# Kernel optimization log

Hardware: AMD Instinct MI355X
Metric: run time of the kernel (lower is better)

The kernel has to match this reference:

```python
import jax, jax.numpy as jnp
import numpy as np

N, H, W, C = 4, 128, 128, 128
G = 8
GC = C // G
K = 9  # 3x3 deformable kernel
PAD = 1
HIN, WIN = H + 2 * PAD, W + 2 * PAD
EPS = 1e-5
OFFSET_SCALE = 1.0


def ln(x, g, b):
    m = jnp.mean(x, -1, keepdims=True)
    v = jnp.mean((x - m) ** 2, -1, keepdims=True)
    return (x - m) * jax.lax.rsqrt(v + EPS) * g + b


def gelu(x):
    return jax.nn.gelu(x, approximate=False)


def dcn_core(xp, offset, mask):
    # xp: (N,H,W,C) value features; offset: (N,H,W,G*K*2); mask: (N,H,W,G,K)
    xpad = jnp.pad(xp, ((0, 0), (PAD, PAD), (PAD, PAD), (0, 0)))
    img = xpad.reshape(N, HIN * WIN, G, GC)
    # reference points normalized by padded size (matches dcnv3_core_pytorch)
    ref_x = (jnp.arange(W, dtype=jnp.float32) + 1.5) / WIN  # (dil*(k-1))//2 + 0.5
    ref_y = (jnp.arange(H, dtype=jnp.float32) + 1.5) / HIN
    RX, RY = jnp.meshgrid(ref_x, ref_y)  # (H,W), xy indexing
    ref = jnp.stack([RX, RY], -1)  # (H,W,2) as (x,y)
    gx, gy = jnp.meshgrid(jnp.linspace(-1.0, 1.0, 3), jnp.linspace(-1.0, 1.0, 3), indexing='ij')
    grid = jnp.stack([gx / WIN, gy / HIN], -1).reshape(K, 2)  # dilation grid, x-major
    off = offset.reshape(N, H, W, G, K, 2)
    loc = (ref[None, :, :, None, None, :] + grid * OFFSET_SCALE
           + off * OFFSET_SCALE / jnp.array([WIN, HIN], jnp.float32))  # (N,H,W,G,K,2)
    # grid_sample align_corners=False pixel coords
    px = loc[..., 0] * WIN - 0.5
    py = loc[..., 1] * HIN - 0.5
    x0 = jnp.floor(px); y0 = jnp.floor(py)
    tx = px - x0; ty = py - y0
    x0i = x0.astype(jnp.int32); y0i = y0.astype(jnp.int32)
    x1i = x0i + 1; y1i = y0i + 1

    def gather(iy, ix):
        valid = ((iy >= 0) & (iy < HIN) & (ix >= 0) & (ix < WIN)).astype(xp.dtype)
        idx = jnp.clip(iy, 0, HIN - 1) * WIN + jnp.clip(ix, 0, WIN - 1)  # (N,H,W,G,K)
        idxf = idx.transpose(0, 1, 2, 4, 3).reshape(N, H * W * K, G, 1)
        v = jnp.take_along_axis(img, idxf, axis=1).reshape(N, H, W, K, G, GC)
        return v * valid.transpose(0, 1, 2, 4, 3)[..., None]

    acc = jnp.zeros((N, H, W, G, GC), xp.dtype)
    for iy, ix, wgt in ((y0i, x0i, (1 - ty) * (1 - tx)),
                        (y0i, x1i, (1 - ty) * tx),
                        (y1i, x0i, ty * (1 - tx)),
                        (y1i, x1i, ty * tx)):
        wm = (wgt * mask).transpose(0, 1, 2, 4, 3)[..., None]  # (N,H,W,K,G,1)
        acc = acc + jnp.sum(gather(iy, ix) * wm, axis=3)  # (N,H,W,G,GC)
    return acc.reshape(N, H, W, C)


def dcn(x, in_w, in_b, dw_k, dw_b, dwln_g, dwln_b, off_w, off_b, mask_w, mask_b, out_w, out_b):
    xp = x @ in_w + in_b  # input_proj
    # offset/mask branch: depthwise 3x3 conv on raw input, LN, GELU
    xc = jax.lax.conv_general_dilated(
        x, dw_k.reshape(3, 3, 1, C), (1, 1), 'SAME',
        dimension_numbers=('NHWC', 'HWIO', 'NHWC'), feature_group_count=C) + dw_b
    x1 = gelu(ln(xc, dwln_g, dwln_b))
    offset = x1 @ off_w + off_b  # (N,H,W,G*K*2)
    mask = jax.nn.softmax((x1 @ mask_w + mask_b).reshape(N, H, W, G, K), axis=-1)
    y = dcn_core(xp, offset, mask)
    return y @ out_w + out_b


def _forward(x, ln1_g, ln1_b, in_w, in_b, dw_k, dw_b, dwln_g, dwln_b, off_w, off_b,
             mask_w, mask_b, out_w, out_b, ln2_g, ln2_b, fc1_w, fc1_b, fc2_w, fc2_b):
    # pre-norm, no layer_scale, no drop_path (rate 0)
    x = x + dcn(ln(x, ln1_g, ln1_b), in_w, in_b, dw_k, dw_b, dwln_g, dwln_b,
                off_w, off_b, mask_w, mask_b, out_w, out_b)
    h = ln(x, ln2_g, ln2_b)
    h = gelu(h @ fc1_w + fc1_b) @ fc2_w + fc2_b
    return x + h


def setup_inputs() -> dict:
    key = jax.random.key(0)
    ks = jax.random.split(key, 10)

    def lin(k, fin, fout, scale=1.0):
        s = scale / np.sqrt(fin)
        return jax.random.uniform(k, (fin, fout), minval=-s, maxval=s, dtype=jnp.float32)

    d = {}
    d['x'] = jax.random.normal(ks[0], (N, H, W, C), dtype=jnp.float32)
    d['ln1_g'] = jnp.ones((C,), jnp.float32); d['ln1_b'] = jnp.zeros((C,), jnp.float32)
    d['in_w'] = lin(ks[1], C, C); d['in_b'] = jnp.zeros((C,), jnp.float32)
    d['dw_k'] = jax.random.normal(ks[2], (3, 3, C), dtype=jnp.float32) * 0.05
    d['dw_b'] = jnp.zeros((C,), jnp.float32)
    d['dwln_g'] = jnp.ones((C,), jnp.float32); d['dwln_b'] = jnp.zeros((C,), jnp.float32)
    d['off_w'] = lin(ks[3], C, G * K * 2, 0.1); d['off_b'] = jnp.zeros((G * K * 2,), jnp.float32)
    d['mask_w'] = lin(ks[4], C, G * K, 0.1); d['mask_b'] = jnp.zeros((G * K,), jnp.float32)
    d['out_w'] = lin(ks[5], C, C); d['out_b'] = jnp.zeros((C,), jnp.float32)
    d['ln2_g'] = jnp.ones((C,), jnp.float32); d['ln2_b'] = jnp.zeros((C,), jnp.float32)
    d['fc1_w'] = lin(ks[6], C, 4 * C); d['fc1_b'] = jnp.zeros((4 * C,), jnp.float32)
    d['fc2_w'] = lin(ks[7], 4 * C, C); d['fc2_b'] = jnp.zeros((C,), jnp.float32)
    return d


def reference(x, ln1_g, ln1_b, in_w, in_b, dw_k, dw_b, dwln_g, dwln_b, off_w, off_b,
              mask_w, mask_b, out_w, out_b, ln2_g, ln2_b, fc1_w, fc1_b, fc2_w, fc2_b):
    return _forward(x, ln1_g, ln1_b, in_w, in_b, dw_k, dw_b, dwln_g, dwln_b, off_w, off_b,
                    mask_w, mask_b, out_w, out_b, ln2_g, ln2_b, fc1_w, fc1_b, fc2_w, fc2_b)
```

## Files before the change

kernel.cpp:

```cpp
#include <hip/hip_runtime.h>
#include <hip/hip_bf16.h>
#include <math.h>

#define NB 4
#define HH 128
#define WW 128
#define CC 128
#define GG 8
#define GCC 16
#define KK 9
#define NHW (NB*HH*WW)

typedef __hip_bfloat16 bf16;
typedef __attribute__((ext_vector_type(8))) short short8;
typedef __attribute__((ext_vector_type(4))) float f32x4;

__device__ __forceinline__ float b2f(bf16 v){ return __bfloat162float(v); }
__device__ __forceinline__ bf16 f2b(float v){ return __float2bfloat16(v); }
__device__ __forceinline__ float gelu_f(float v){ return 0.5f*v*(1.f+erff(v*0.70710678118654752f)); }
__device__ __forceinline__ float lo_bf(unsigned u){ union{unsigned i; float f;} c; c.i = u<<16; return c.f; }
__device__ __forceinline__ float hi_bf(unsigned u){ union{unsigned i; float f;} c; c.i = u&0xffff0000u; return c.f; }
__device__ __forceinline__ unsigned pk(float a, float b){
  return ((unsigned)__bfloat16_as_ushort(f2b(b))<<16) | (unsigned)__bfloat16_as_ushort(f2b(a));
}
__device__ __forceinline__ void st_out(bf16* p, float v){ *p = f2b(v); }
__device__ __forceinline__ void st_out(float* p, float v){ *p = v; }
__device__ __forceinline__ void acc8(float* a, uint4 u, float w){
  a[0]+=w*lo_bf(u.x); a[1]+=w*hi_bf(u.x); a[2]+=w*lo_bf(u.y); a[3]+=w*hi_bf(u.y);
  a[4]+=w*lo_bf(u.z); a[5]+=w*hi_bf(u.z); a[6]+=w*lo_bf(u.w); a[7]+=w*hi_bf(u.w);
}

__global__ __launch_bounds__(256) void prep_k(
    const float* __restrict__ inw,  const float* __restrict__ outw,
    const float* __restrict__ fc1w, const float* __restrict__ fc2w,
    const float* __restrict__ offw, const float* __restrict__ offb,
    const float* __restrict__ maskw,const float* __restrict__ maskb,
    bf16* __restrict__ inwt, bf16* __restrict__ outwt,
    bf16* __restrict__ w1t,  bf16* __restrict__ w2t,
    bf16* __restrict__ wsw,  float* __restrict__ cw)
{
  int idx = blockIdx.x*256 + threadIdx.x;
  if (idx < 16384){
    int n = idx>>7, k = idx&127;
    inwt[idx] = f2b(inw[(size_t)k*128 + n]);
  } else if (idx < 32768){
    int i = idx-16384; int n = i>>7, k = i&127;
    outwt[i] = f2b(outw[(size_t)k*128 + n]);
  } else if (idx < 98304){
    int i = idx-32768; int n = i>>7, k = i&127;
    w1t[i] = f2b(fc1w[(size_t)k*512 + n]);
  } else if (idx < 163840){
    int i = idx-98304; int n = i>>9, k = i&511;
    w2t[i] = f2b(fc2w[(size_t)k*128 + n]);
  } else if (idx < 192512){
    int i = idx-163840; int nn = i>>7, k = i&127;
    float v = (nn<144) ? offw[(size_t)k*144+nn] : (nn<216 ? maskw[(size_t)k*72+(nn-144)] : 0.f);
    wsw[i] = f2b(v);
  } else if (idx < 192736){
    int i = idx-192512;
    cw[i] = (i<144) ? offb[i] : (i<216 ? maskb[i-144] : 0.f);
  }
}

__global__ __launch_bounds__(256) void ln_k(const float* __restrict__ X,
    const float* __restrict__ gam, const float* __restrict__ bet, bf16* __restrict__ Y)
{
  int lane = threadIdx.x & 63;
  int wid  = threadIdx.x >> 6;
  size_t pix = (size_t)blockIdx.x*4 + wid;
  const float* xp = X + pix*CC;
  int c0 = lane*2;
  float v0 = xp[c0], v1 = xp[c0+1];
  float s = v0+v1, ss = v0*v0+v1*v1;
  #pragma unroll
  for (int off=32; off>0; off>>=1){ s += __shfl_xor(s,off,64); ss += __shfl_xor(ss,off,64); }
  float mean = s*(1.f/CC);
  float var  = ss*(1.f/CC) - mean*mean;
  float rstd = rsqrtf(var + 1e-5f);
  float y0 = (v0-mean)*rstd*gam[c0]   + bet[c0];
  float y1 = (v1-mean)*rstd*gam[c0+1] + bet[c0+1];
  Y[pix*CC + c0]   = f2b(y0);
  Y[pix*CC + c0+1] = f2b(y1);
}

__global__ __launch_bounds__(256) void convln_k(const bf16* __restrict__ XN,
    const float* __restrict__ dwk, const float* __restrict__ dwb,
    const float* __restrict__ gam, const float* __restrict__ bet, bf16* __restrict__ X1)
{
  int tid = threadIdx.x;
  int px = tid>>4, cg = tid&15;
  int ch0 = cg*8;
  int pix = blockIdx.x*16 + px;
  int w = pix & (WW-1), h = (pix>>7)&(HH-1), n = pix>>14;
  float acc[8];
  {
    float4 b0 = *(const float4*)(dwb + ch0), b1 = *(const float4*)(dwb + ch0 + 4);
    acc[0]=b0.x; acc[1]=b0.y; acc[2]=b0.z; acc[3]=b0.w;
    acc[4]=b1.x; acc[5]=b1.y; acc[6]=b1.z; acc[7]=b1.w;
  }
  #pragma unroll
  for (int ky=0;ky<3;ky++){
    int yy = h+ky-1; if ((unsigned)yy>=(unsigned)HH) continue;
    #pragma unroll
    for (int kx=0;kx<3;kx++){
      int xx = w+kx-1; if ((unsigned)xx>=(unsigned)WW) continue;
      uint4 u = *(const uint4*)(XN + ((size_t)((n*HH+yy)*WW+xx))*CC + ch0);
      const float* wp = dwk + (ky*3+kx)*CC + ch0;
      float4 w0 = *(const float4*)wp; float4 w1 = *(const float4*)(wp+4);
      acc[0] += lo_bf(u.x)*w0.x; acc[1] += hi_bf(u.x)*w0.y;
      acc[2] += lo_bf(u.y)*w0.z; acc[3] += hi_bf(u.y)*w0.w;
      acc[4] += lo_bf(u.z)*w1.x; acc[5] += hi_bf(u.z)*w1.y;
      acc[6] += lo_bf(u.w)*w1.z; acc[7] += hi_bf(u.w)*w1.w;
    }
  }
  float s=0.f, ss=0.f;
  #pragma unroll
  for (int i=0;i<8;i++){ s += acc[i]; ss += acc[i]*acc[i]; }
  #pragma unroll
  for (int off=1; off<16; off<<=1){ s += __shfl_xor(s,off,64); ss += __shfl_xor(ss,off,64); }
  float mean=s*(1.f/CC), var=ss*(1.f/CC)-mean*mean, rstd=rsqrtf(var+1e-5f);
  float4 g0 = *(const float4*)(gam + ch0), g1 = *(const float4*)(gam + ch0 + 4);
  float4 be0 = *(const float4*)(bet + ch0), be1 = *(const float4*)(bet + ch0 + 4);
  float gv[8] = {g0.x,g0.y,g0.z,g0.w,g1.x,g1.y,g1.z,g1.w};
  float bv[8] = {be0.x,be0.y,be0.z,be0.w,be1.x,be1.y,be1.z,be1.w};
  float o[8];
  #pragma unroll
  for (int i=0;i<8;i++) o[i] = gelu_f((acc[i]-mean)*rstd*gv[i] + bv[i]);
  uint4 up; up.x = pk(o[0],o[1]); up.y = pk(o[2],o[3]); up.z = pk(o[4],o[5]); up.w = pk(o[6],o[7]);
  *(uint4*)(X1 + (size_t)pix*CC + ch0) = up;
}

#define OMS 226
__global__ __launch_bounds__(256) void samp_k(const bf16* __restrict__ X1,
    const bf16* __restrict__ XP,
    const bf16* __restrict__ wsw, const float* __restrict__ cw,
    bf16* __restrict__ Y)
{
  __shared__ bf16 oms[32*OMS];
  int tid = threadIdx.x;
  int pix0 = blockIdx.x*32;
  int wave = tid>>6, l = tid&63, lo16 = l&15, quad = l>>4;
  int nt0 = wave*4;
  int ntn = (wave==3) ? 2 : 4;
  short8 af[2][4];
  #pragma unroll
  for (int mt=0;mt<2;mt++)
    #pragma unroll
    for (int ks=0;ks<4;ks++)
      af[mt][ks] = *(const short8*)(X1 + (size_t)(pix0+mt*16+lo16)*128 + ks*32 + quad*8);
  f32x4 z = {0.f,0.f,0.f,0.f};
  f32x4 acc[2][4];
  #pragma unroll
  for (int mt=0;mt<2;mt++)
    #pragma unroll
    for (int t=0;t<4;t++) acc[mt][t]=z;
  for (int t=0;t<ntn;t++){
    int nt = nt0+t;
    #pragma unroll
    for (int ks=0;ks<4;ks++){
      short8 bfr = *(const short8*)(wsw + (size_t)(nt*16+lo16)*128 + ks*32 + quad*8);
      acc[0][t] = __builtin_amdgcn_mfma_f32_16x16x32_bf16(af[0][ks], bfr, acc[0][t], 0,0,0);
      acc[1][t] = __builtin_amdgcn_mfma_f32_16x16x32_bf16(af[1][ks], bfr, acc[1][t], 0,0,0);
    }
  }
  for (int t=0;t<ntn;t++){
    int col = (nt0+t)*16 + lo16;
    float bb = cw[col];
    #pragma unroll
    for (int mt=0;mt<2;mt++)
      #pragma unroll
      for (int r=0;r<4;r++)
        oms[(mt*16 + quad*4 + r)*OMS + col] = f2b(acc[mt][t][r] + bb);
  }
  __syncthreads();
  {
    int m = tid>>3, g = tid&7;
    int base = m*OMS + 144 + g*9;
    float sc[9]; float mx = -1e30f;
    #pragma unroll
    for (int k=0;k<9;k++){ sc[k] = b2f(oms[base+k]); mx = fmaxf(mx, sc[k]); }
    float sum = 0.f;
    #pragma unroll
    for (int k=0;k<9;k++){ sc[k] = expf(sc[k]-mx); sum += sc[k]; }
    float inv = 1.f/sum;
    #pragma unroll
    for (int k=0;k<9;k++) oms[base+k] = f2b(sc[k]*inv);
  }
  __syncthreads();
  int oct = tid&15, sl = tid>>4;
  int g = oct>>1;
  int ch = g*GCC + (oct&1)*8;
  int w0 = pix0 & (WW-1);
  int h  = (pix0>>7) & (HH-1);
  int n  = pix0>>14;
  const bf16* base = XP + (size_t)n*HH*WW*CC + ch;
  for (int it=0; it<2; it++){
    int m = it*16 + sl;
    int wc = w0 + m;
    const bf16* omrow = &oms[m*OMS];
    float a[8] = {0.f,0.f,0.f,0.f,0.f,0.f,0.f,0.f};
    #pragma unroll
    for (int k=0;k<9;k++){
      float offx = b2f(omrow[g*18 + 2*k]);
      float offy = b2f(omrow[g*18 + 2*k + 1]);
      float mk   = b2f(omrow[144 + g*9 + k]);
      float pxf = (float)(wc + (k/3) - 1) + offx;
      float pyf = (float)(h  + (k%3) - 1) + offy;
      float x0f = floorf(pxf), y0f = floorf(pyf);
      float txf = pxf-x0f,     tyf = pyf-y0f;
      int x0 = (int)x0f, y0 = (int)y0f;
      int x1i = x0+1,    y1i = y0+1;
      float vx0 = ((unsigned)x0 <(unsigned)WW)?1.f:0.f;
      float vx1 = ((unsigned)x1i<(unsigned)WW)?1.f:0.f;
      float vy0 = ((unsigned)y0 <(unsigned)HH)?1.f:0.f;
      float vy1 = ((unsigned)y1i<(unsigned)HH)?1.f:0.f;
      int cx0 = min(max(x0,0),WW-1),  cx1 = min(max(x1i,0),WW-1);
      int cy0 = min(max(y0,0),HH-1),  cy1 = min(max(y1i,0),HH-1);
      float w00=(1.f-tyf)*(1.f-txf)*mk*vy0*vx0, w01=(1.f-tyf)*txf*mk*vy0*vx1;
      float w10=tyf*(1.f-txf)*mk*vy1*vx0,       w11=tyf*txf*mk*vy1*vx1;
      uint4 u00 = *(const uint4*)(base + ((size_t)(cy0*WW+cx0))*CC);
      uint4 u01 = *(const uint4*)(base + ((size_t)(cy0*WW+cx1))*CC);
      uint4 u10 = *(const uint4*)(base + ((size_t)(cy1*WW+cx0))*CC);
      uint4 u11 = *(const uint4*)(base + ((size_t)(cy1*WW+cx1))*CC);
      acc8(a,u00,w00); acc8(a,u01,w01); acc8(a,u10,w10); acc8(a,u11,w11);
    }
    uint4 outp;
    outp.x = pk(a[0],a[1]); outp.y = pk(a[2],a[3]);
    outp.z = pk(a[4],a[5]); outp.w = pk(a[6],a[7]);
    *(uint4*)(Y + (size_t)(pix0+m)*CC + ch) = outp;
  }
}

template<typename OutT, bool RES>
__global__ __launch_bounds__(256) void gemm_mfma(const bf16* __restrict__ A,
    const bf16* __restrict__ Bt, const float* __restrict__ bias,
    const float* __restrict__ res, OutT* __restrict__ C)
{
  int tid = threadIdx.x;
  int wave = tid>>6, l = tid&63, lo16 = l&15, quad = l>>4;
  int m0 = blockIdx.y*256 + wave*64;
  int n0 = blockIdx.x*64;
  short8 bfr[4][4];
  #pragma unroll
  for (int ks=0;ks<4;ks++)
    #pragma unroll
    for (int nt=0;nt<4;nt++)
      bfr[ks][nt] = *(const short8*)(Bt + (size_t)(n0+nt*16+lo16)*128 + ks*32 + quad*8);
  f32x4 z = {0.f,0.f,0.f,0.f};
  f32x4 acc[4][4];
  #pragma unroll
  for (int mt=0;mt<4;mt++)
    #pragma unroll
    for (int nt=0;nt<4;nt++) acc[mt][nt]=z;
  #pragma unroll
  for (int ks=0;ks<4;ks++){
    short8 af[4];
    #pragma unroll
    for (int mt=0;mt<4;mt++)
      af[mt] = *(const short8*)(A + (size_t)(m0+mt*16+lo16)*128 + ks*32 + quad*8);
    #pragma unroll
    for (int nt=0;nt<4;nt++)
      #pragma unroll
      for (int mt=0;mt<4;mt++)
        acc[mt][nt] = __builtin_amdgcn_mfma_f32_16x16x32_bf16(af[mt], bfr[ks][nt], acc[mt][nt], 0,0,0);
  }
  #pragma unroll
  for (int mt=0;mt<4;mt++)
    #pragma unroll
    for (int nt=0;nt<4;nt++){
      int col = n0 + nt*16 + lo16;
      float bb = bias[col];
      #pragma unroll
      for (int r=0;r<4;r++){
        int row = m0 + mt*16 + quad*4 + r;
        float v = acc[mt][nt][r] + bb;
        if (RES) v += res[(size_t)row*128 + col];
        st_out(&C[(size_t)row*128 + col], v);
      }
    }
}

__global__ __launch_bounds__(256) void mlp_mfma(const float* __restrict__ X2,
    const float* __restrict__ lng, const float* __restrict__ lnb,
    const bf16* __restrict__ w1t, const float* __restrict__ b1,
    const bf16* __restrict__ w2t, const float* __restrict__ b2,
    float* __restrict__ OUT)
{
  __shared__ __align__(16) char smem[34816 + 18432];
  bf16* h0s = (bf16*)smem;
  bf16* ts  = (bf16*)smem;
  bf16* w1s = (bf16*)(smem + 34816);
  bf16* w2s = (bf16*)(smem + 34816);
  int tid = threadIdx.x;
  int wave = tid>>6, l = tid&63, lo16 = l&15, quad = l>>4;
  int m0 = blockIdx.x*128;
  #pragma unroll
  for (int itn=0; itn<2; itn++){
    int px = (tid>>2) + itn*64;
    int q = tid&3;
    const float* xr = X2 + (size_t)(m0+px)*128 + q*32;
    float v[32];
    #pragma unroll
    for (int i=0;i<8;i++) *(float4*)(v+i*4) = *(const float4*)(xr+i*4);
    float s=0.f, ss=0.f;
    #pragma unroll
    for (int i=0;i<32;i++){ s += v[i]; ss += v[i]*v[i]; }
    s  += __shfl_xor(s,1,64);  ss += __shfl_xor(ss,1,64);
    s  += __shfl_xor(s,2,64);  ss += __shfl_xor(ss,2,64);
    float mean = s*(1.f/CC), var = ss*(1.f/CC)-mean*mean, rstd = rsqrtf(var+1e-5f);
    const float* gp = lng + q*32; const float* bp = lnb + q*32;
    uint4* dst = (uint4*)(&h0s[px*136 + q*32]);
    #pragma unroll
    for (int i=0;i<4;i++){
      float4 g0 = *(const float4*)(gp+i*8),  g1 = *(const float4*)(gp+i*8+4);
      float4 c0v = *(const float4*)(bp+i*8), c1v = *(const float4*)(bp+i*8+4);
      float o0 = (v[i*8+0]-mean)*rstd*g0.x + c0v.x;
      float o1 = (v[i*8+1]-mean)*rstd*g0.y + c0v.y;
      float o2 = (v[i*8+2]-mean)*rstd*g0.z + c0v.z;
      float o3 = (v[i*8+3]-mean)*rstd*g0.w + c0v.w;
      float o4 = (v[i*8+4]-mean)*rstd*g1.x + c1v.x;
      float o5 = (v[i*8+5]-mean)*rstd*g1.y + c1v.y;
      float o6 = (v[i*8+6]-mean)*rstd*g1.z + c1v.z;
      float o7 = (v[i*8+7]-mean)*rstd*g1.w + c1v.w;
      uint4 up; up.x = pk(o0,o1); up.y = pk(o2,o3); up.z = pk(o4,o5); up.w = pk(o6,o7);
      dst[i] = up;
    }
  }
  __syncthreads();
  short8 a1[2][4];
  #pragma unroll
  for (int mt=0;mt<2;mt++)
    #pragma unroll
    for (int ks=0;ks<4;ks++)
      a1[mt][ks] = *(const short8*)(&h0s[(wave*32 + mt*16 + lo16)*136 + ks*32 + quad*8]);
  f32x4 z = {0.f,0.f,0.f,0.f};
  f32x4 acc2[2][8];
  #pragma unroll
  for (int mt=0;mt<2;mt++)
    #pragma unroll
    for (int nt=0;nt<8;nt++) acc2[mt][nt]=z;

  for (int c0=0;c0<512;c0+=64){
    __syncthreads();
    #pragma unroll
    for (int it=0;it<4;it++){
      int e = it*2048 + tid*8;
      int nn = e>>7, kk = e&127;
      *(uint4*)(&w1s[nn*136 + kk]) = *(const uint4*)(w1t + (size_t)(c0+nn)*128 + kk);
    }
    __syncthreads();
    f32x4 acc1[2][4];
    #pragma unroll
    for (int mt=0;mt<2;mt++)
      #pragma unroll
      for (int nt=0;nt<4;nt++) acc1[mt][nt]=z;
    #pragma unroll
    for (int ks=0;ks<4;ks++)
      #pragma unroll
      for (int nt=0;nt<4;nt++){
        short8 bfr = *(const short8*)(&w1s[(nt*16+lo16)*136 + ks*32 + quad*8]);
        acc1[0][nt] = __builtin_amdgcn_mfma_f32_16x16x32_bf16(a1[0][ks], bfr, acc1[0][nt], 0,0,0);
        acc1[1][nt] = __builtin_amdgcn_mfma_f32_16x16x32_bf16(a1[1][ks], bfr, acc1[1][nt], 0,0,0);
      }
    #pragma unroll
    for (int mt=0;mt<2;mt++)
      #pragma unroll
      for (int nt=0;nt<4;nt++){
        float bb = b1[c0 + nt*16 + lo16];
        #pragma unroll
        for (int r=0;r<4;r++)
          ts[(wave*32 + mt*16 + quad*4 + r)*72 + nt*16 + lo16] = f2b(gelu_f(acc1[mt][nt][r] + bb));
      }
    __syncthreads();
    #pragma unroll
    for (int it=0;it<4;it++){
      int e = it*2048 + tid*8;
      int nn = e>>6, kk = e&63;
      *(uint4*)(&w2s[nn*72 + kk]) = *(const uint4*)(w2t + (size_t)nn*512 + c0 + kk);
    }
    __syncthreads();
    #pragma unroll
    for (int ks2=0;ks2<2;ks2++){
      short8 a2[2];
      #pragma unroll
      for (int mt=0;mt<2;mt++)
        a2[mt] = *(const short8*)(&ts[(wave*32 + mt*16 + lo16)*72 + ks2*32 + quad*8]);
      #pragma unroll
      for (int nt2=0;nt2<8;nt2++){
        short8 bfr2 = *(const short8*)(&w2s[(nt2*16+lo16)*72 + ks2*32 + quad*8]);
        acc2[0][nt2] = __builtin_amdgcn_mfma_f32_16x16x32_bf16(a2[0], bfr2, acc2[0][nt2], 0,0,0);
        acc2[1][nt2] = __builtin_amdgcn_mfma_f32_16x16x32_bf16(a2[1], bfr2, acc2[1][nt2], 0,0,0);
      }
    }
  }
  #pragma unroll
  for (int mt=0;mt<2;mt++)
    #pragma unroll
    for (int nt=0;nt<8;nt++){
      int col = nt*16 + lo16;
      float bb = b2[col];
      #pragma unroll
      for (int r=0;r<4;r++){
        int row = m0 + wave*32 + mt*16 + quad*4 + r;
        float v = acc2[mt][nt][r] + bb + X2[(size_t)row*128 + col];
        OUT[(size_t)row*128 + col] = v;
      }
    }
}

extern "C" void kernel_launch(void* const* d_in, const int* in_sizes, int n_in,
                              void* d_out, int out_size, void* d_ws, size_t ws_size,
                              hipStream_t stream)
{
  const float* x    = (const float*)d_in[0];
  const float* ln1g = (const float*)d_in[1];
  const float* ln1b = (const float*)d_in[2];
  const float* inw  = (const float*)d_in[3];
  const float* inb  = (const float*)d_in[4];
  const float* dwk  = (const float*)d_in[5];
  const float* dwb  = (const float*)d_in[6];
  const float* dwlng= (const float*)d_in[7];
  const float* dwlnb= (const float*)d_in[8];
  const float* offw = (const float*)d_in[9];
  const float* offb = (const float*)d_in[10];
  const float* maskw= (const float*)d_in[11];
  const float* maskb= (const float*)d_in[12];
  const float* outw = (const float*)d_in[13];
  const float* outb = (const float*)d_in[14];
  const float* ln2g = (const float*)d_in[15];
  const float* ln2b = (const float*)d_in[16];
  const float* fc1w = (const float*)d_in[17];
  const float* fc1b = (const float*)d_in[18];
  const float* fc2w = (const float*)d_in[19];
  const float* fc2b = (const float*)d_in[20];
  float* out = (float*)d_out;

  bf16* ws = (bf16*)d_ws;
  const size_t S = (size_t)NHW*CC;
  bf16* xn = ws;
  bf16* xp = ws + S;
  bf16* x1 = ws + 2*S;
  bf16* y  = xn;
  float* x2 = out;
  bf16* inwt  = ws + 3*S;
  bf16* outwt = inwt + 128*128;
  bf16* w1t   = outwt + 128*128;
  bf16* w2t   = w1t + 512*128;
  bf16* wsw   = w2t + 128*512;
  float* cw   = (float*)(wsw + 224*128);

  prep_k<<<753, 256, 0, stream>>>(inw, outw, fc1w, fc2w, offw, offb, maskw, maskb,
                                  inwt, outwt, w1t, w2t, wsw, cw);
  ln_k<<<NHW/4, 256, 0, stream>>>(x, ln1g, ln1b, xn);
  gemm_mfma<bf16,false><<<dim3(2,256), 256, 0, stream>>>(xn, inwt, inb, nullptr, xp);
  convln_k<<<NHW/16, 256, 0, stream>>>(xn, dwk, dwb, dwlng, dwlnb, x1);
  samp_k<<<NHW/32, 256, 0, stream>>>(x1, xp, wsw, cw, y);
  gemm_mfma<float,true><<<dim3(2,256), 256, 0, stream>>>(y, outwt, outb, x, x2);
  mlp_mfma<<<NHW/128, 256, 0, stream>>>(x2, ln2g, ln2b, w1t, fc1b, w2t, fc2b, out);
}
```

Before: 284.5 us.

## Prefetch MLP weight chunks into registers and use polynomial erf GELU

In the MLP kernel, the next 64-column chunks of both fc1 and fc2 weights are loaded from global memory into registers while the current chunk is being computed. Both chunks are stored into shared memory together, which removes one of the two per-chunk barrier rounds. The shared-memory layout is repacked, the hidden-activation row stride shrinks to 68, and launch bounds ask for two blocks per SM. GELU's erff is replaced by an Abramowitz-Stegun polynomial using fast rcp and exp, trading a little accuracy for cheaper math. The new row stride is not a multiple of 16 bytes, so the 16-byte LDS reads may be misaligned. Carrying the prefetched weights in registers also adds register pressure.

```diff
diff --git a/kernel.cpp b/kernel.cpp
--- a/kernel.cpp
+++ b/kernel.cpp
@@ -17,7 +17,15 @@
 
 __device__ __forceinline__ float b2f(bf16 v){ return __bfloat162float(v); }
 __device__ __forceinline__ bf16 f2b(float v){ return __float2bfloat16(v); }
-__device__ __forceinline__ float gelu_f(float v){ return 0.5f*v*(1.f+erff(v*0.70710678118654752f)); }
+__device__ __forceinline__ float gelu_f(float v){
+  float x = fabsf(v) * 0.70710678118654752f;
+  float t = __builtin_amdgcn_rcpf(fmaf(0.3275911f, x, 1.0f));
+  float p = t*fmaf(t, fmaf(t, fmaf(t, fmaf(t, 1.061405429f, -1.453152027f),
+                         1.421413741f), -0.284496736f), 0.254829592f);
+  float e = __expf(-x*x);
+  float er = copysignf(fmaf(-p, e, 1.0f), v);
+  return 0.5f*v*(1.0f+er);
+}
 __device__ __forceinline__ float lo_bf(unsigned u){ union{unsigned i; float f;} c; c.i = u<<16; return c.f; }
 __device__ __forceinline__ float hi_bf(unsigned u){ union{unsigned i; float f;} c; c.i = u&0xffff0000u; return c.f; }
 __device__ __forceinline__ unsigned pk(float a, float b){
@@ -280,20 +288,28 @@
     }
 }
 
-__global__ __launch_bounds__(256) void mlp_mfma(const float* __restrict__ X2,
+__global__ __launch_bounds__(256, 2) void mlp_mfma(const float* __restrict__ X2,
     const float* __restrict__ lng, const float* __restrict__ lnb,
     const bf16* __restrict__ w1t, const float* __restrict__ b1,
     const bf16* __restrict__ w2t, const float* __restrict__ b2,
     float* __restrict__ OUT)
 {
-  __shared__ __align__(16) char smem[34816 + 18432];
+  __shared__ __align__(16) char smem[53248];
   bf16* h0s = (bf16*)smem;
   bf16* ts  = (bf16*)smem;
-  bf16* w1s = (bf16*)(smem + 34816);
+  bf16* w1s = (bf16*)(smem + 17408);
   bf16* w2s = (bf16*)(smem + 34816);
   int tid = threadIdx.x;
   int wave = tid>>6, l = tid&63, lo16 = l&15, quad = l>>4;
   int m0 = blockIdx.x*128;
+  int t8 = tid*8;
+  uint4 pw1[4], pw2[4];
+  #pragma unroll
+  for (int it=0;it<4;it++){
+    int e = it*2048 + t8;
+    pw1[it] = *(const uint4*)(w1t + (size_t)(e>>7)*128 + (e&127));
+    pw2[it] = *(const uint4*)(w2t + (size_t)(e>>6)*512 + (e&63));
+  }
   #pragma unroll
   for (int itn=0; itn<2; itn++){
     int px = (tid>>2) + itn*64;
@@ -344,9 +360,18 @@
     __syncthreads();
     #pragma unroll
     for (int it=0;it<4;it++){
-      int e = it*2048 + tid*8;
-      int nn = e>>7, kk = e&127;
-      *(uint4*)(&w1s[nn*136 + kk]) = *(const uint4*)(w1t + (size_t)(c0+nn)*128 + kk);
+      int e = it*2048 + t8;
+      *(uint4*)(&w1s[(e>>7)*136 + (e&127)]) = pw1[it];
+      *(uint4*)(&w2s[(e>>6)*72 + (e&63)]) = pw2[it];
+    }
+    if (c0 < 448){
+      int c1 = c0 + 64;
+      #pragma unroll
+      for (int it=0;it<4;it++){
+        int e = it*2048 + t8;
+        pw1[it] = *(const uint4*)(w1t + (size_t)(c1 + (e>>7))*128 + (e&127));
+        pw2[it] = *(const uint4*)(w2t + (size_t)(e>>6)*512 + c1 + (e&63));
+      }
     }
     __syncthreads();
     f32x4 acc1[2][4];
@@ -369,22 +394,15 @@
         float bb = b1[c0 + nt*16 + lo16];
         #pragma unroll
         for (int r=0;r<4;r++)
-          ts[(wave*32 + mt*16 + quad*4 + r)*72 + nt*16 + lo16] = f2b(gelu_f(acc1[mt][nt][r] + bb));
-      }
-    __syncthreads();
-    #pragma unroll
-    for (int it=0;it<4;it++){
-      int e = it*2048 + tid*8;
-      int nn = e>>6, kk = e&63;
-      *(uint4*)(&w2s[nn*72 + kk]) = *(const uint4*)(w2t + (size_t)nn*512 + c0 + kk);
-    }
+          ts[(wave*32 + mt*16 + quad*4 + r)*68 + nt*16 + lo16] = f2b(gelu_f(acc1[mt][nt][r] + bb));
+      }
     __syncthreads();
     #pragma unroll
     for (int ks2=0;ks2<2;ks2++){
       short8 a2[2];
       #pragma unroll
       for (int mt=0;mt<2;mt++)
-        a2[mt] = *(const short8*)(&ts[(wave*32 + mt*16 + lo16)*72 + ks2*32 + quad*8]);
+        a2[mt] = *(const short8*)(&ts[(wave*32 + mt*16 + lo16)*68 + ks2*32 + quad*8]);
       #pragma unroll
       for (int nt2=0;nt2<8;nt2++){
         short8 bfr2 = *(const short8*)(&w2s[(nt2*16+lo16)*72 + ks2*32 + quad*8]);
```

Measured after the change: 299.3 us. 5.2% more time.
